# Kernel optimization log

Hardware: AMD Instinct MI355X
Metric: run time of the kernel (lower is better)

The kernel has to match this reference:

```python
import jax, jax.numpy as jnp
import numpy as np

EPS = 1e-5  # BatchNorm eps (torch default)


def setup_inputs() -> dict:
    key = jax.random.key(0)
    ks = jax.random.split(key, 12)
    C, Ci, B, H, W = 64, 32, 2, 96, 96  # plane, inter_plane=plane//2

    def n(k, shape, s=0.05):
        return jax.random.normal(k, shape, jnp.float32) * s

    return {
        "xA": jax.random.normal(ks[0], (B, C, H, W), jnp.float32),
        "xB": jax.random.normal(ks[1], (B, C, H, W), jnp.float32),
        "Wk": n(ks[2], (Ci, C)), "bk": n(ks[3], (Ci,)),
        "Wv": n(ks[4], (Ci, C)), "bv": n(ks[5], (Ci,)),
        "Wq": n(ks[6], (Ci, C)), "bq": n(ks[7], (Ci,)),
        "Wg": n(ks[8], (Ci, Ci)),  # conv_wg, 1x1 Conv1d, no bias
        "g1_gamma": jnp.ones((Ci,), jnp.float32), "g1_beta": jnp.zeros((Ci,), jnp.float32),
        "g1_mean": jnp.zeros((Ci,), jnp.float32), "g1_var": jnp.ones((Ci,), jnp.float32),
        "Wo": n(ks[9], (C, Ci)), "bo": n(ks[10], (C,)),
        "g2_gamma": jnp.ones((C,), jnp.float32), "g2_beta": jnp.zeros((C,), jnp.float32),
        "g2_mean": jnp.zeros((C,), jnp.float32), "g2_var": jnp.ones((C,), jnp.float32),
    }


def reference(xA, xB, Wk, bk, Wv, bv, Wq, bq, Wg,
              g1_gamma, g1_beta, g1_mean, g1_var,
              Wo, bo, g2_gamma, g2_beta, g2_mean, g2_var):
    B, C, H, W = xB.shape
    N = H * W
    # 1x1 conv2d projections -> [B, Ci, N]
    k = (jnp.einsum('bchw,oc->bohw', xA, Wk) + bk[None, :, None, None]).reshape(B, -1, N)
    v = (jnp.einsum('bchw,oc->bohw', xA, Wv) + bv[None, :, None, None]).reshape(B, -1, N)
    q = (jnp.einsum('bchw,oc->bohw', xB, Wq) + bq[None, :, None, None]).reshape(B, -1, N)
    # AV = softmax(v^T @ q, axis=2)  -> [B, N, N]
    A = jax.nn.softmax(jnp.einsum('bcn,bcm->bnm', v, q), axis=2)
    # k @ AV -> [B, Ci, N]
    av = jnp.einsum('bcn,bnm->bcm', k, A)
    # conv_wg (1x1 conv1d, no bias) + BatchNorm1d (inference form)
    av = jnp.einsum('oc,bcn->bon', Wg, av)
    av = (av - g1_mean[None, :, None]) * (g1_gamma / jnp.sqrt(g1_var + EPS))[None, :, None] + g1_beta[None, :, None]
    av = av.reshape(B, -1, H, W)
    # out: 1x1 conv2d -> plane, BatchNorm2d, residual, relu
    o = jnp.einsum('oc,bchw->bohw', Wo, av) + bo[None, :, None, None]
    o = (o - g2_mean[None, :, None, None]) * (g2_gamma / jnp.sqrt(g2_var + EPS))[None, :, None, None] + g2_beta[None, :, None, None]
    return jax.nn.relu(o + xB)
```

## Files before the change

kernel.cpp:

```cpp
#include <hip/hip_runtime.h>
#include <hip/hip_bf16.h>

#define CI 32
#define CC 64
#define NBATCH 2
#define NPIX 9216
#define NSA 8
#define NSD 16
#define LOG2E 1.4426950408889634f

typedef __attribute__((ext_vector_type(8))) short s16x8;
typedef __attribute__((ext_vector_type(4))) float f32x4;
typedef __attribute__((ext_vector_type(2))) unsigned int u32x2;
typedef __attribute__((ext_vector_type(4))) unsigned int u32x4;

static __device__ __forceinline__ unsigned cvtpk(float a, float b) {
    unsigned d;
    asm("v_cvt_pk_bf16_f32 %0, %1, %2" : "=v"(d) : "v"(a), "v"(b));
    return d;
}
static __device__ __forceinline__ short f2b(float f) {
    union { float f; unsigned u; } v; v.f = f;
    return (short)((v.u + 0x7FFFu + ((v.u >> 16) & 1u)) >> 16);
}
static __device__ __forceinline__ float b2f(short s) {
    union { unsigned u; float f; } v; v.u = ((unsigned)(unsigned short)s) << 16;
    return v.f;
}

__global__ __launch_bounds__(128) void k_proj(
    const float* __restrict__ xA, const float* __restrict__ xB,
    const float* __restrict__ Wk, const float* __restrict__ bk,
    const float* __restrict__ Wv, const float* __restrict__ bv,
    const float* __restrict__ Wq, const float* __restrict__ bq,
    short* __restrict__ vT, short* __restrict__ qT, short* __restrict__ kC)
{
    int mode = blockIdx.y;
    const float* W    = mode == 0 ? Wk : (mode == 1 ? Wv : Wq);
    const float* bias = mode == 0 ? bk : (mode == 1 ? bv : bq);
    const float* X    = mode == 2 ? xB : xA;

    __shared__ float sW[CI * CC];
    __shared__ float sb[CI];
    for (int i = threadIdx.x; i < CI * CC; i += 128) sW[i] = W[i];
    if (threadIdx.x < CI) sb[threadIdx.x] = bias[threadIdx.x];
    __syncthreads();

    int idx = blockIdx.x * 128 + threadIdx.x;
    int b = idx / NPIX, n = idx % NPIX;

    float acc[CI];
    #pragma unroll
    for (int o = 0; o < CI; o++) acc[o] = sb[o];

    const float* px = X + (size_t)b * CC * NPIX + n;
    for (int c = 0; c < CC; c++) {
        float x = px[(size_t)c * NPIX];
        #pragma unroll
        for (int o = 0; o < CI; o++) acc[o] += sW[o * CC + c] * x;
    }

    if (mode == 0) {
        #pragma unroll
        for (int o = 0; o < CI; o++)
            kC[((size_t)b * CI + o) * NPIX + n] = f2b(acc[o]);
    } else {
        float sc = (mode == 2) ? LOG2E : 1.0f;
        short* dst = (mode == 1 ? vT : qT) + ((size_t)b * NPIX + n) * CI;
        #pragma unroll
        for (int q4 = 0; q4 < 4; q4++) {
            u32x4 pk;
            #pragma unroll
            for (int j = 0; j < 4; j++)
                pk[j] = cvtpk(acc[q4 * 8 + 2 * j] * sc, acc[q4 * 8 + 2 * j + 1] * sc);
            ((u32x4*)dst)[q4] = pk;
        }
    }
}

__global__ __launch_bounds__(128) void k_denom(
    const short* __restrict__ vT, const short* __restrict__ qT,
    float* __restrict__ sum_part)
{
    int w = threadIdx.x >> 6, lane = threadIdx.x & 63;
    int r = lane & 15, g = lane >> 4;
    int b = blockIdx.y;
    int nb = blockIdx.x * 64 + w * 32;

    const short* vb = vT + (size_t)b * NPIX * CI;
    s16x8 a0 = *(const s16x8*)(vb + (size_t)(nb + r) * CI + 8 * g);
    s16x8 a1 = *(const s16x8*)(vb + (size_t)(nb + 16 + r) * CI + 8 * g);

    f32x4 s0 = {0.f, 0.f, 0.f, 0.f}, s1 = {0.f, 0.f, 0.f, 0.f};
    f32x4 z  = {0.f, 0.f, 0.f, 0.f};
    const short* qb = qT + (size_t)b * NPIX * CI;
    int mlo = blockIdx.z * (NPIX / NSD);
    int mhi = mlo + NPIX / NSD;
    for (int m0 = mlo; m0 < mhi; m0 += 32) {
        s16x8 q0 = *(const s16x8*)(qb + (size_t)(m0 + r) * CI + 8 * g);
        s16x8 q1 = *(const s16x8*)(qb + (size_t)(m0 + 16 + r) * CI + 8 * g);
        f32x4 t00 = __builtin_amdgcn_mfma_f32_16x16x32_bf16(a0, q0, z, 0, 0, 0);
        f32x4 t01 = __builtin_amdgcn_mfma_f32_16x16x32_bf16(a0, q1, z, 0, 0, 0);
        f32x4 t10 = __builtin_amdgcn_mfma_f32_16x16x32_bf16(a1, q0, z, 0, 0, 0);
        f32x4 t11 = __builtin_amdgcn_mfma_f32_16x16x32_bf16(a1, q1, z, 0, 0, 0);
        #pragma unroll
        for (int e = 0; e < 4; e++) {
            s0[e] += __builtin_amdgcn_exp2f(t00[e]) + __builtin_amdgcn_exp2f(t01[e]);
            s1[e] += __builtin_amdgcn_exp2f(t10[e]) + __builtin_amdgcn_exp2f(t11[e]);
        }
    }
    #pragma unroll
    for (int mask = 1; mask < 16; mask <<= 1) {
        #pragma unroll
        for (int e = 0; e < 4; e++) {
            s0[e] += __shfl_xor(s0[e], mask, 64);
            s1[e] += __shfl_xor(s1[e], mask, 64);
        }
    }
    if (r == 0) {
        float* sp = sum_part + ((size_t)blockIdx.z * NBATCH + b) * NPIX;
        #pragma unroll
        for (int e = 0; e < 4; e++) {
            sp[nb + 4 * g + e]      = s0[e];
            sp[nb + 16 + 4 * g + e] = s1[e];
        }
    }
}

__global__ __launch_bounds__(256) void k_l2d(
    const float* __restrict__ sum_part, float* __restrict__ nl2d)
{
    int idx = blockIdx.x * 256 + threadIdx.x;
    float s = 0.f;
    #pragma unroll
    for (int zz = 0; zz < NSD; zz++)
        s += sum_part[(size_t)zz * NBATCH * NPIX + idx];
    nl2d[idx] = -__builtin_amdgcn_logf(s);
}

__global__ __launch_bounds__(128) void k_attn(
    const short* __restrict__ vT, const short* __restrict__ qT,
    const short* __restrict__ kC, const float* __restrict__ nl2d,
    short* __restrict__ avp)
{
    __shared__ __align__(16) short plds[2][32][40];
    int w = threadIdx.x >> 6, lane = threadIdx.x & 63;
    int r = lane & 15, g = lane >> 4;
    int b = blockIdx.y;
    int m0 = blockIdx.x * 64 + w * 32;

    const short* qb = qT + (size_t)b * NPIX * CI;
    s16x8 qb0 = *(const s16x8*)(qb + (size_t)(m0 + r) * CI + 8 * g);
    s16x8 qb1 = *(const s16x8*)(qb + (size_t)(m0 + 16 + r) * CI + 8 * g);

    const short* vb = vT + (size_t)b * NPIX * CI;
    const short* k0 = kC + ((size_t)b * CI + r) * NPIX;
    const short* k1 = k0 + (size_t)16 * NPIX;
    const float* nl2 = nl2d + (size_t)b * NPIX;

    f32x4 acc00 = {0,0,0,0}, acc01 = {0,0,0,0}, acc10 = {0,0,0,0}, acc11 = {0,0,0,0};

    int nlo = blockIdx.z * (NPIX / NSA);
    int nhi = nlo + NPIX / NSA;
    for (int n0 = nlo; n0 < nhi; n0 += 32) {
        f32x4 c0 = *(const f32x4*)(nl2 + n0 + 4 * g);
        f32x4 c1 = *(const f32x4*)(nl2 + n0 + 16 + 4 * g);
        s16x8 a0 = *(const s16x8*)(vb + (size_t)(n0 + r) * CI + 8 * g);
        s16x8 a1 = *(const s16x8*)(vb + (size_t)(n0 + 16 + r) * CI + 8 * g);

        f32x4 t00 = __builtin_amdgcn_mfma_f32_16x16x32_bf16(a0, qb0, c0, 0, 0, 0);
        f32x4 t01 = __builtin_amdgcn_mfma_f32_16x16x32_bf16(a0, qb1, c0, 0, 0, 0);
        f32x4 t10 = __builtin_amdgcn_mfma_f32_16x16x32_bf16(a1, qb0, c1, 0, 0, 0);
        f32x4 t11 = __builtin_amdgcn_mfma_f32_16x16x32_bf16(a1, qb1, c1, 0, 0, 0);

        u32x2 w00 = {cvtpk(__builtin_amdgcn_exp2f(t00[0]), __builtin_amdgcn_exp2f(t00[1])),
                     cvtpk(__builtin_amdgcn_exp2f(t00[2]), __builtin_amdgcn_exp2f(t00[3]))};
        u32x2 w10 = {cvtpk(__builtin_amdgcn_exp2f(t10[0]), __builtin_amdgcn_exp2f(t10[1])),
                     cvtpk(__builtin_amdgcn_exp2f(t10[2]), __builtin_amdgcn_exp2f(t10[3]))};
        u32x2 w01 = {cvtpk(__builtin_amdgcn_exp2f(t01[0]), __builtin_amdgcn_exp2f(t01[1])),
                     cvtpk(__builtin_amdgcn_exp2f(t01[2]), __builtin_amdgcn_exp2f(t01[3]))};
        u32x2 w11 = {cvtpk(__builtin_amdgcn_exp2f(t11[0]), __builtin_amdgcn_exp2f(t11[1])),
                     cvtpk(__builtin_amdgcn_exp2f(t11[2]), __builtin_amdgcn_exp2f(t11[3]))};

        *(u32x2*)&plds[w][r][4 * g]           = w00;
        *(u32x2*)&plds[w][r][16 + 4 * g]      = w10;
        *(u32x2*)&plds[w][16 + r][4 * g]      = w01;
        *(u32x2*)&plds[w][16 + r][16 + 4 * g] = w11;

        s16x8 pb0 = *(const s16x8*)&plds[w][r][8 * g];
        s16x8 pb1 = *(const s16x8*)&plds[w][16 + r][8 * g];
        s16x8 ka0 = *(const s16x8*)(k0 + n0 + 8 * g);
        s16x8 ka1 = *(const s16x8*)(k1 + n0 + 8 * g);

        acc00 = __builtin_amdgcn_mfma_f32_16x16x32_bf16(ka0, pb0, acc00, 0, 0, 0);
        acc10 = __builtin_amdgcn_mfma_f32_16x16x32_bf16(ka1, pb0, acc10, 0, 0, 0);
        acc01 = __builtin_amdgcn_mfma_f32_16x16x32_bf16(ka0, pb1, acc01, 0, 0, 0);
        acc11 = __builtin_amdgcn_mfma_f32_16x16x32_bf16(ka1, pb1, acc11, 0, 0, 0);
    }

    short* dst = avp + ((size_t)blockIdx.z * NBATCH + b) * NPIX * CI;
    u32x2 o00 = {cvtpk(acc00[0], acc00[1]), cvtpk(acc00[2], acc00[3])};
    u32x2 o10 = {cvtpk(acc10[0], acc10[1]), cvtpk(acc10[2], acc10[3])};
    u32x2 o01 = {cvtpk(acc01[0], acc01[1]), cvtpk(acc01[2], acc01[3])};
    u32x2 o11 = {cvtpk(acc11[0], acc11[1]), cvtpk(acc11[2], acc11[3])};
    *(u32x2*)(dst + (size_t)(m0 + r) * CI + 4 * g)           = o00;
    *(u32x2*)(dst + (size_t)(m0 + r) * CI + 16 + 4 * g)      = o10;
    *(u32x2*)(dst + (size_t)(m0 + 16 + r) * CI + 4 * g)      = o01;
    *(u32x2*)(dst + (size_t)(m0 + 16 + r) * CI + 16 + 4 * g) = o11;
}

__global__ __launch_bounds__(64) void k_e1(
    const short* __restrict__ avp, const float* __restrict__ Wg,
    const float* __restrict__ g1g, const float* __restrict__ g1b,
    const float* __restrict__ g1m, const float* __restrict__ g1v,
    short* __restrict__ a2buf)
{
    __shared__ float sWg[CI * CI], s1[CI], t1[CI];
    int t = threadIdx.x;
    for (int i = t; i < CI * CI; i += 64) sWg[i] = Wg[i];
    if (t < CI) {
        float s = g1g[t] * rsqrtf(g1v[t] + 1e-5f);
        s1[t] = s; t1[t] = g1b[t] - g1m[t] * s;
    }
    __syncthreads();

    int idx = blockIdx.x * 64 + t;
    float a[CI];
    #pragma unroll
    for (int c = 0; c < CI; c++) a[c] = 0.f;
    #pragma unroll
    for (int zz = 0; zz < NSA; zz++) {
        const short* p = avp + ((size_t)zz * NBATCH * NPIX + idx) * CI;
        #pragma unroll
        for (int v8 = 0; v8 < 4; v8++) {
            s16x8 tv = *(const s16x8*)(p + 8 * v8);
            #pragma unroll
            for (int j = 0; j < 8; j++) a[8 * v8 + j] += b2f(tv[j]);
        }
    }
    float a2[CI];
    #pragma unroll
    for (int o = 0; o < CI; o++) {
        float acc = 0.f;
        #pragma unroll
        for (int c = 0; c < CI; c++) acc += sWg[o * CI + c] * a[c];
        a2[o] = acc * s1[o] + t1[o];
    }
    short* dst = a2buf + (size_t)idx * CI;
    #pragma unroll
    for (int q4 = 0; q4 < 4; q4++) {
        u32x4 pk;
        #pragma unroll
        for (int j = 0; j < 4; j++)
            pk[j] = cvtpk(a2[q4 * 8 + 2 * j], a2[q4 * 8 + 2 * j + 1]);
        ((u32x4*)dst)[q4] = pk;
    }
}

__global__ __launch_bounds__(64) void k_e2(
    const short* __restrict__ a2buf,
    const float* __restrict__ Wo, const float* __restrict__ bo,
    const float* __restrict__ g2g, const float* __restrict__ g2b,
    const float* __restrict__ g2m, const float* __restrict__ g2v,
    const float* __restrict__ xB, float* __restrict__ out)
{
    __shared__ float sWo[32 * CI], s2[32], t2[32];
    int t = threadIdx.x, jh = blockIdx.y;
    for (int i = t; i < 32 * CI; i += 64) sWo[i] = Wo[jh * 32 * CI + i];
    if (t < 32) {
        int j = jh * 32 + t;
        float s = g2g[j] * rsqrtf(g2v[j] + 1e-5f);
        s2[t] = s; t2[t] = g2b[j] - g2m[j] * s + bo[j] * s;
    }
    __syncthreads();

    int idx = blockIdx.x * 64 + t;
    int b = idx / NPIX, m = idx % NPIX;

    float a2[CI];
    const short* p = a2buf + (size_t)idx * CI;
    #pragma unroll
    for (int v8 = 0; v8 < 4; v8++) {
        s16x8 tv = *(const s16x8*)(p + 8 * v8);
        #pragma unroll
        for (int j = 0; j < 8; j++) a2[8 * v8 + j] = b2f(tv[j]);
    }
    #pragma unroll
    for (int jj = 0; jj < 32; jj++) {
        float acc = 0.f;
        #pragma unroll
        for (int o = 0; o < CI; o++) acc += sWo[jj * CI + o] * a2[o];
        acc = acc * s2[jj] + t2[jj];
        size_t oi = ((size_t)b * CC + jh * 32 + jj) * NPIX + m;
        float res = acc + xB[oi];
        out[oi] = res > 0.f ? res : 0.f;
    }
}

extern "C" void kernel_launch(void* const* d_in, const int* in_sizes, int n_in,
                              void* d_out, int out_size, void* d_ws, size_t ws_size,
                              hipStream_t stream)
{
    const float* xA = (const float*)d_in[0];
    const float* xB = (const float*)d_in[1];
    const float* Wk = (const float*)d_in[2];
    const float* bk = (const float*)d_in[3];
    const float* Wv = (const float*)d_in[4];
    const float* bv = (const float*)d_in[5];
    const float* Wq = (const float*)d_in[6];
    const float* bq = (const float*)d_in[7];
    const float* Wg = (const float*)d_in[8];
    const float* g1g = (const float*)d_in[9];
    const float* g1b = (const float*)d_in[10];
    const float* g1m = (const float*)d_in[11];
    const float* g1v = (const float*)d_in[12];
    const float* Wo = (const float*)d_in[13];
    const float* bo = (const float*)d_in[14];
    const float* g2g = (const float*)d_in[15];
    const float* g2b = (const float*)d_in[16];
    const float* g2m = (const float*)d_in[17];
    const float* g2v = (const float*)d_in[18];
    float* out = (float*)d_out;

    char* ws = (char*)d_ws;
    const size_t SZB = (size_t)NBATCH * NPIX * CI * 2;
    short* vT = (short*)(ws);
    short* qT = (short*)(ws + SZB);
    short* kC = (short*)(ws + 2 * SZB);
    float* nl2d = (float*)(ws + 3 * SZB);
    char*  region = ws + 3 * SZB + (size_t)NBATCH * NPIX * 4;
    float* sum_part = (float*)region;
    short* avp = (short*)region;
    short* a2buf = vT;

    k_proj<<<dim3(NBATCH * NPIX / 128, 3), dim3(128), 0, stream>>>(
        xA, xB, Wk, bk, Wv, bv, Wq, bq, vT, qT, kC);
    k_denom<<<dim3(NPIX / 64, NBATCH, NSD), dim3(128), 0, stream>>>(
        vT, qT, sum_part);
    k_l2d<<<dim3(NBATCH * NPIX / 256), dim3(256), 0, stream>>>(
        sum_part, nl2d);
    k_attn<<<dim3(NPIX / 64, NBATCH, NSA), dim3(128), 0, stream>>>(
        vT, qT, kC, nl2d, avp);
    k_e1<<<dim3(NBATCH * NPIX / 64), dim3(64), 0, stream>>>(
        avp, Wg, g1g, g1b, g1m, g1v, a2buf);
    k_e2<<<dim3(NBATCH * NPIX / 64, 2), dim3(64), 0, stream>>>(
        a2buf, Wo, bo, g2g, g2b, g2m, g2v, xB, out);
}
```

Baseline: 154.4 us.

## Fold softmax denominator into K, split projection channels, fuse epilogue kernels

The softmax normalisation moves out of the attention loop. Instead of adding -log(denominator) as the MFMA accumulator init, the reciprocal denominator now pre-scales kC in a new elementwise kernel, so the first MFMAs start from zero and the per-iteration nl2d loads disappear. The projection kernel splits the 64 input channels across four wavefronts and reduces the partial sums through LDS. The attention split count becomes 16 when the workspace is large enough, the partial reduction becomes a separate vectorised kernel, and the Wg/BN1 and Wo/BN2/residual stages are fused into one kernel. Rounding pre-scaled K to bf16 changes numerics, and the extra kernels add launch and memory passes.

```diff
diff --git a/kernel.cpp b/kernel.cpp
--- a/kernel.cpp
+++ b/kernel.cpp
@@ -5,11 +5,11 @@
 #define CC 64
 #define NBATCH 2
 #define NPIX 9216
-#define NSA 8
 #define NSD 16
 #define LOG2E 1.4426950408889634f
 
 typedef __attribute__((ext_vector_type(8))) short s16x8;
+typedef __attribute__((ext_vector_type(4))) short s16x4;
 typedef __attribute__((ext_vector_type(4))) float f32x4;
 typedef __attribute__((ext_vector_type(2))) unsigned int u32x2;
 typedef __attribute__((ext_vector_type(4))) unsigned int u32x4;
@@ -28,7 +28,7 @@
     return v.f;
 }
 
-__global__ __launch_bounds__(128) void k_proj(
+__global__ __launch_bounds__(256) void k_proj(
     const float* __restrict__ xA, const float* __restrict__ xB,
     const float* __restrict__ Wk, const float* __restrict__ bk,
     const float* __restrict__ Wv, const float* __restrict__ bv,
@@ -42,38 +42,52 @@
 
     __shared__ float sW[CI * CC];
     __shared__ float sb[CI];
-    for (int i = threadIdx.x; i < CI * CC; i += 128) sW[i] = W[i];
+    __shared__ float spart[3][64][33];
+    for (int i = threadIdx.x; i < CI * CC; i += 256) sW[i] = W[i];
     if (threadIdx.x < CI) sb[threadIdx.x] = bias[threadIdx.x];
     __syncthreads();
 
-    int idx = blockIdx.x * 128 + threadIdx.x;
+    int q4 = threadIdx.x >> 6;
+    int lp = threadIdx.x & 63;
+    int idx = blockIdx.x * 64 + lp;
     int b = idx / NPIX, n = idx % NPIX;
 
     float acc[CI];
     #pragma unroll
-    for (int o = 0; o < CI; o++) acc[o] = sb[o];
+    for (int o = 0; o < CI; o++) acc[o] = 0.f;
 
     const float* px = X + (size_t)b * CC * NPIX + n;
-    for (int c = 0; c < CC; c++) {
+    #pragma unroll
+    for (int cc = 0; cc < 16; cc++) {
+        int c = q4 * 16 + cc;
         float x = px[(size_t)c * NPIX];
         #pragma unroll
         for (int o = 0; o < CI; o++) acc[o] += sW[o * CC + c] * x;
     }
-
-    if (mode == 0) {
+    if (q4) {
+        #pragma unroll
+        for (int o = 0; o < CI; o++) spart[q4 - 1][lp][o] = acc[o];
+    }
+    __syncthreads();
+    if (q4 == 0) {
         #pragma unroll
         for (int o = 0; o < CI; o++)
-            kC[((size_t)b * CI + o) * NPIX + n] = f2b(acc[o]);
-    } else {
-        float sc = (mode == 2) ? LOG2E : 1.0f;
-        short* dst = (mode == 1 ? vT : qT) + ((size_t)b * NPIX + n) * CI;
-        #pragma unroll
-        for (int q4 = 0; q4 < 4; q4++) {
-            u32x4 pk;
+            acc[o] += spart[0][lp][o] + spart[1][lp][o] + spart[2][lp][o] + sb[o];
+        if (mode == 0) {
             #pragma unroll
-            for (int j = 0; j < 4; j++)
-                pk[j] = cvtpk(acc[q4 * 8 + 2 * j] * sc, acc[q4 * 8 + 2 * j + 1] * sc);
-            ((u32x4*)dst)[q4] = pk;
+            for (int o = 0; o < CI; o++)
+                kC[((size_t)b * CI + o) * NPIX + n] = f2b(acc[o]);
+        } else {
+            float sc = (mode == 2) ? LOG2E : 1.0f;
+            short* dst = (mode == 1 ? vT : qT) + ((size_t)b * NPIX + n) * CI;
+            #pragma unroll
+            for (int v4 = 0; v4 < 4; v4++) {
+                u32x4 pk;
+                #pragma unroll
+                for (int j = 0; j < 4; j++)
+                    pk[j] = cvtpk(acc[v4 * 8 + 2 * j] * sc, acc[v4 * 8 + 2 * j + 1] * sc);
+                ((u32x4*)dst)[v4] = pk;
+            }
         }
     }
 }
@@ -127,23 +141,31 @@
     }
 }
 
-__global__ __launch_bounds__(256) void k_l2d(
-    const float* __restrict__ sum_part, float* __restrict__ nl2d)
+__global__ __launch_bounds__(256) void k_invd(
+    const float* __restrict__ sum_part, float* __restrict__ invd)
 {
     int idx = blockIdx.x * 256 + threadIdx.x;
     float s = 0.f;
     #pragma unroll
     for (int zz = 0; zz < NSD; zz++)
         s += sum_part[(size_t)zz * NBATCH * NPIX + idx];
-    nl2d[idx] = -__builtin_amdgcn_logf(s);
+    invd[idx] = 1.0f / s;
+}
+
+__global__ __launch_bounds__(256) void k_scale(
+    short* __restrict__ kC, const float* __restrict__ invd)
+{
+    int idx = blockIdx.x * 256 + threadIdx.x;
+    int n = idx % NPIX;
+    int b = idx / (CI * NPIX);
+    kC[idx] = f2b(b2f(kC[idx]) * invd[b * NPIX + n]);
 }
 
 __global__ __launch_bounds__(128) void k_attn(
     const short* __restrict__ vT, const short* __restrict__ qT,
-    const short* __restrict__ kC, const float* __restrict__ nl2d,
-    short* __restrict__ avp)
-{
-    __shared__ __align__(16) short plds[2][32][40];
+    const short* __restrict__ kC, short* __restrict__ avp, int slice)
+{
+    __shared__ short plds[2][32][36];
     int w = threadIdx.x >> 6, lane = threadIdx.x & 63;
     int r = lane & 15, g = lane >> 4;
     int b = blockIdx.y;
@@ -156,22 +178,22 @@
     const short* vb = vT + (size_t)b * NPIX * CI;
     const short* k0 = kC + ((size_t)b * CI + r) * NPIX;
     const short* k1 = k0 + (size_t)16 * NPIX;
-    const float* nl2 = nl2d + (size_t)b * NPIX;
 
     f32x4 acc00 = {0,0,0,0}, acc01 = {0,0,0,0}, acc10 = {0,0,0,0}, acc11 = {0,0,0,0};
-
-    int nlo = blockIdx.z * (NPIX / NSA);
-    int nhi = nlo + NPIX / NSA;
+    f32x4 z = {0,0,0,0};
+
+    int nlo = blockIdx.z * slice;
+    int nhi = nlo + slice;
     for (int n0 = nlo; n0 < nhi; n0 += 32) {
-        f32x4 c0 = *(const f32x4*)(nl2 + n0 + 4 * g);
-        f32x4 c1 = *(const f32x4*)(nl2 + n0 + 16 + 4 * g);
-        s16x8 a0 = *(const s16x8*)(vb + (size_t)(n0 + r) * CI + 8 * g);
-        s16x8 a1 = *(const s16x8*)(vb + (size_t)(n0 + 16 + r) * CI + 8 * g);
-
-        f32x4 t00 = __builtin_amdgcn_mfma_f32_16x16x32_bf16(a0, qb0, c0, 0, 0, 0);
-        f32x4 t01 = __builtin_amdgcn_mfma_f32_16x16x32_bf16(a0, qb1, c0, 0, 0, 0);
-        f32x4 t10 = __builtin_amdgcn_mfma_f32_16x16x32_bf16(a1, qb0, c1, 0, 0, 0);
-        f32x4 t11 = __builtin_amdgcn_mfma_f32_16x16x32_bf16(a1, qb1, c1, 0, 0, 0);
+        s16x8 a0  = *(const s16x8*)(vb + (size_t)(n0 + r) * CI + 8 * g);
+        s16x8 a1  = *(const s16x8*)(vb + (size_t)(n0 + 16 + r) * CI + 8 * g);
+        s16x8 ka0 = *(const s16x8*)(k0 + n0 + 8 * g);
+        s16x8 ka1 = *(const s16x8*)(k1 + n0 + 8 * g);
+
+        f32x4 t00 = __builtin_amdgcn_mfma_f32_16x16x32_bf16(a0, qb0, z, 0, 0, 0);
+        f32x4 t01 = __builtin_amdgcn_mfma_f32_16x16x32_bf16(a0, qb1, z, 0, 0, 0);
+        f32x4 t10 = __builtin_amdgcn_mfma_f32_16x16x32_bf16(a1, qb0, z, 0, 0, 0);
+        f32x4 t11 = __builtin_amdgcn_mfma_f32_16x16x32_bf16(a1, qb1, z, 0, 0, 0);
 
         u32x2 w00 = {cvtpk(__builtin_amdgcn_exp2f(t00[0]), __builtin_amdgcn_exp2f(t00[1])),
                      cvtpk(__builtin_amdgcn_exp2f(t00[2]), __builtin_amdgcn_exp2f(t00[3]))};
@@ -187,10 +209,12 @@
         *(u32x2*)&plds[w][16 + r][4 * g]      = w01;
         *(u32x2*)&plds[w][16 + r][16 + 4 * g] = w11;
 
-        s16x8 pb0 = *(const s16x8*)&plds[w][r][8 * g];
-        s16x8 pb1 = *(const s16x8*)&plds[w][16 + r][8 * g];
-        s16x8 ka0 = *(const s16x8*)(k0 + n0 + 8 * g);
-        s16x8 ka1 = *(const s16x8*)(k1 + n0 + 8 * g);
+        s16x4 l0 = *(const s16x4*)&plds[w][r][8 * g];
+        s16x4 h0 = *(const s16x4*)&plds[w][r][8 * g + 4];
+        s16x4 l1 = *(const s16x4*)&plds[w][16 + r][8 * g];
+        s16x4 h1 = *(const s16x4*)&plds[w][16 + r][8 * g + 4];
+        s16x8 pb0 = {l0[0], l0[1], l0[2], l0[3], h0[0], h0[1], h0[2], h0[3]};
+        s16x8 pb1 = {l1[0], l1[1], l1[2], l1[3], h1[0], h1[1], h1[2], h1[3]};
 
         acc00 = __builtin_amdgcn_mfma_f32_16x16x32_bf16(ka0, pb0, acc00, 0, 0, 0);
         acc10 = __builtin_amdgcn_mfma_f32_16x16x32_bf16(ka1, pb0, acc10, 0, 0, 0);
@@ -209,81 +233,67 @@
     *(u32x2*)(dst + (size_t)(m0 + 16 + r) * CI + 16 + 4 * g) = o11;
 }
 
-__global__ __launch_bounds__(64) void k_e1(
-    const short* __restrict__ avp, const float* __restrict__ Wg,
+__global__ __launch_bounds__(256) void e_red(
+    const short* __restrict__ avp, short* __restrict__ av, int nsa)
+{
+    int vecidx = blockIdx.x * 256 + threadIdx.x;
+    const short* src = avp + (size_t)vecidx * 8;
+    float s[8];
+    #pragma unroll
+    for (int j = 0; j < 8; j++) s[j] = 0.f;
+    for (int zz = 0; zz < nsa; zz++) {
+        s16x8 t = *(const s16x8*)(src + (size_t)zz * NBATCH * NPIX * CI);
+        #pragma unroll
+        for (int j = 0; j < 8; j++) s[j] += b2f(t[j]);
+    }
+    u32x4 pk;
+    #pragma unroll
+    for (int j = 0; j < 4; j++) pk[j] = cvtpk(s[2 * j], s[2 * j + 1]);
+    *(u32x4*)(av + (size_t)vecidx * 8) = pk;
+}
+
+__global__ __launch_bounds__(256) void e_fused(
+    const short* __restrict__ av,
+    const float* __restrict__ Wg,
     const float* __restrict__ g1g, const float* __restrict__ g1b,
     const float* __restrict__ g1m, const float* __restrict__ g1v,
-    short* __restrict__ a2buf)
-{
-    __shared__ float sWg[CI * CI], s1[CI], t1[CI];
-    int t = threadIdx.x;
-    for (int i = t; i < CI * CI; i += 64) sWg[i] = Wg[i];
-    if (t < CI) {
-        float s = g1g[t] * rsqrtf(g1v[t] + 1e-5f);
-        s1[t] = s; t1[t] = g1b[t] - g1m[t] * s;
-    }
-    __syncthreads();
-
-    int idx = blockIdx.x * 64 + t;
-    float a[CI];
-    #pragma unroll
-    for (int c = 0; c < CI; c++) a[c] = 0.f;
-    #pragma unroll
-    for (int zz = 0; zz < NSA; zz++) {
-        const short* p = avp + ((size_t)zz * NBATCH * NPIX + idx) * CI;
-        #pragma unroll
-        for (int v8 = 0; v8 < 4; v8++) {
-            s16x8 tv = *(const s16x8*)(p + 8 * v8);
-            #pragma unroll
-            for (int j = 0; j < 8; j++) a[8 * v8 + j] += b2f(tv[j]);
-        }
-    }
-    float a2[CI];
-    #pragma unroll
-    for (int o = 0; o < CI; o++) {
-        float acc = 0.f;
-        #pragma unroll
-        for (int c = 0; c < CI; c++) acc += sWg[o * CI + c] * a[c];
-        a2[o] = acc * s1[o] + t1[o];
-    }
-    short* dst = a2buf + (size_t)idx * CI;
-    #pragma unroll
-    for (int q4 = 0; q4 < 4; q4++) {
-        u32x4 pk;
-        #pragma unroll
-        for (int j = 0; j < 4; j++)
-            pk[j] = cvtpk(a2[q4 * 8 + 2 * j], a2[q4 * 8 + 2 * j + 1]);
-        ((u32x4*)dst)[q4] = pk;
-    }
-}
-
-__global__ __launch_bounds__(64) void k_e2(
-    const short* __restrict__ a2buf,
     const float* __restrict__ Wo, const float* __restrict__ bo,
     const float* __restrict__ g2g, const float* __restrict__ g2b,
     const float* __restrict__ g2m, const float* __restrict__ g2v,
     const float* __restrict__ xB, float* __restrict__ out)
 {
-    __shared__ float sWo[32 * CI], s2[32], t2[32];
+    __shared__ float sWg[CI * CI], sWo[32 * CI], s1[CI], t1[CI], s2[32], t2[32];
     int t = threadIdx.x, jh = blockIdx.y;
-    for (int i = t; i < 32 * CI; i += 64) sWo[i] = Wo[jh * 32 * CI + i];
-    if (t < 32) {
-        int j = jh * 32 + t;
+    for (int i = t; i < CI * CI; i += 256) sWg[i] = Wg[i];
+    for (int i = t; i < 32 * CI; i += 256) sWo[i] = Wo[jh * 32 * CI + i];
+    if (t < CI) {
+        float s = g1g[t] * rsqrtf(g1v[t] + 1e-5f);
+        s1[t] = s; t1[t] = g1b[t] - g1m[t] * s;
+    } else if (t < CI + 32) {
+        int j = jh * 32 + (t - CI);
         float s = g2g[j] * rsqrtf(g2v[j] + 1e-5f);
-        s2[t] = s; t2[t] = g2b[j] - g2m[j] * s + bo[j] * s;
+        s2[t - CI] = s; t2[t - CI] = g2b[j] - g2m[j] * s + bo[j] * s;
     }
     __syncthreads();
 
-    int idx = blockIdx.x * 64 + t;
+    int idx = blockIdx.x * 256 + t;
     int b = idx / NPIX, m = idx % NPIX;
 
-    float a2[CI];
-    const short* p = a2buf + (size_t)idx * CI;
+    float a[CI];
+    const short* p = av + (size_t)idx * CI;
     #pragma unroll
     for (int v8 = 0; v8 < 4; v8++) {
         s16x8 tv = *(const s16x8*)(p + 8 * v8);
         #pragma unroll
-        for (int j = 0; j < 8; j++) a2[8 * v8 + j] = b2f(tv[j]);
+        for (int j = 0; j < 8; j++) a[8 * v8 + j] = b2f(tv[j]);
+    }
+    float a2[CI];
+    #pragma unroll
+    for (int o = 0; o < CI; o++) {
+        float acc = 0.f;
+        #pragma unroll
+        for (int c = 0; c < CI; c++) acc += sWg[o * CI + c] * a[c];
+        a2[o] = acc * s1[o] + t1[o];
     }
     #pragma unroll
     for (int jj = 0; jj < 32; jj++) {
@@ -327,22 +337,28 @@
     short* vT = (short*)(ws);
     short* qT = (short*)(ws + SZB);
     short* kC = (short*)(ws + 2 * SZB);
-    float* nl2d = (float*)(ws + 3 * SZB);
+    float* invd = (float*)(ws + 3 * SZB);
     char*  region = ws + 3 * SZB + (size_t)NBATCH * NPIX * 4;
     float* sum_part = (float*)region;
     short* avp = (short*)region;
-    short* a2buf = vT;
-
-    k_proj<<<dim3(NBATCH * NPIX / 128, 3), dim3(128), 0, stream>>>(
+    short* av = vT;
+
+    const size_t base = 3 * SZB + (size_t)NBATCH * NPIX * 4;
+    int nsa = (ws_size >= base + (size_t)16 * NBATCH * NPIX * CI * 2) ? 16 : 8;
+    int slice = NPIX / nsa;
+
+    k_proj<<<dim3(NBATCH * NPIX / 64, 3), dim3(256), 0, stream>>>(
         xA, xB, Wk, bk, Wv, bv, Wq, bq, vT, qT, kC);
     k_denom<<<dim3(NPIX / 64, NBATCH, NSD), dim3(128), 0, stream>>>(
         vT, qT, sum_part);
-    k_l2d<<<dim3(NBATCH * NPIX / 256), dim3(256), 0, stream>>>(
-        sum_part, nl2d);
-    k_attn<<<dim3(NPIX / 64, NBATCH, NSA), dim3(128), 0, stream>>>(
-        vT, qT, kC, nl2d, avp);
-    k_e1<<<dim3(NBATCH * NPIX / 64), dim3(64), 0, stream>>>(
-        avp, Wg, g1g, g1b, g1m, g1v, a2buf);
-    k_e2<<<dim3(NBATCH * NPIX / 64, 2), dim3(64), 0, stream>>>(
-        a2buf, Wo, bo, g2g, g2b, g2m, g2v, xB, out);
-}
+    k_invd<<<dim3(NBATCH * NPIX / 256), dim3(256), 0, stream>>>(
+        sum_part, invd);
+    k_scale<<<dim3(NBATCH * CI * NPIX / 256), dim3(256), 0, stream>>>(
+        kC, invd);
+    k_attn<<<dim3(NPIX / 64, NBATCH, nsa), dim3(128), 0, stream>>>(
+        vT, qT, kC, avp, slice);
+    e_red<<<dim3(NBATCH * NPIX * CI / 8 / 256), dim3(256), 0, stream>>>(
+        avp, av, nsa);
+    e_fused<<<dim3(NBATCH * NPIX / 256, 2), dim3(256), 0, stream>>>(
+        av, Wg, g1g, g1b, g1m, g1v, Wo, bo, g2g, g2b, g2m, g2v, xB, out);
+}
```

New measurement: 140.2 us. -9.2%, faster.
